# Optimization experiments

Measured on AMD Instinct MI355X. Metric: run time of the kernel, lower is better.

Reference implementation:

```python
import jax, jax.numpy as jnp
import numpy as np

N_NODES = 40000
N_EDGES = 640000
IN_FEATS = 256
EDGE_FEATS = 64
OUT_FEATS = 128
NUM_HEADS = 8
D = OUT_FEATS // NUM_HEADS  # 16


def setup_inputs() -> dict:
    key = jax.random.key(0)
    ks = jax.random.split(key, 9)
    node_feats = jax.random.normal(ks[0], (N_NODES, IN_FEATS), dtype=jnp.float32)
    edge_feats = jax.random.normal(ks[1], (N_EDGES, EDGE_FEATS), dtype=jnp.float32)
    src = jax.random.randint(ks[2], (N_EDGES,), 0, N_NODES, dtype=jnp.int32)
    dst = jax.random.randint(ks[3], (N_EDGES,), 0, N_NODES, dtype=jnp.int32)
    # learned parameters (xavier-ish scale)
    node_w = jax.random.normal(ks[4], (OUT_FEATS, IN_FEATS), dtype=jnp.float32) * (2.0 / (IN_FEATS + OUT_FEATS)) ** 0.5
    node_b = jnp.zeros((OUT_FEATS,), dtype=jnp.float32)
    edge_w = jax.random.normal(ks[5], (OUT_FEATS, EDGE_FEATS), dtype=jnp.float32) * (2.0 / (EDGE_FEATS + OUT_FEATS)) ** 0.5
    edge_b = jnp.zeros((OUT_FEATS,), dtype=jnp.float32)
    attn = jax.random.normal(ks[6], (1, NUM_HEADS, 3 * D), dtype=jnp.float32) * 0.1
    return {"node_feats": node_feats, "edge_feats": edge_feats, "src": src, "dst": dst,
            "node_w": node_w, "node_b": node_b, "edge_w": edge_w, "edge_b": edge_b, "attn": attn}


def reference(node_feats, edge_feats, src, dst, node_w, node_b, edge_w, edge_b, attn):
    N = node_feats.shape[0]
    # Node / edge projections -> [N,H,D], [E,H,D]
    Wh = (node_feats @ node_w.T + node_b).reshape(-1, NUM_HEADS, D)
    We = (edge_feats @ edge_w.T + edge_b).reshape(-1, NUM_HEADS, D)
    # Split attn into src/dst/edge parts: attn is [1,H,3D]
    a = attn[0]  # [H,3D]
    a_src, a_dst, a_e = a[:, :D], a[:, D:2 * D], a[:, 2 * D:]
    # Per-node partial scores [N,H], then gather per edge; edge part [E,H]
    s_src = jnp.einsum('nhd,hd->nh', Wh, a_src)
    s_dst = jnp.einsum('nhd,hd->nh', Wh, a_dst)
    s_e = jnp.einsum('ehd,hd->eh', We, a_e)
    e = s_src[src] + s_dst[dst] + s_e  # [E,H]
    e = jax.nn.leaky_relu(e, negative_slope=0.2)
    # Edge softmax over incoming edges of each dst node
    m = jax.ops.segment_max(e, dst, num_segments=N)          # [N,H]
    ex = jnp.exp(e - m[dst])                                  # [E,H]
    z = jax.ops.segment_sum(ex, dst, num_segments=N)          # [N,H]
    alpha = ex / z[dst]                                       # [E,H]
    # Weighted scatter-sum aggregation of source features
    msg = alpha[:, :, None] * Wh[src]                         # [E,H,D]
    h = jax.ops.segment_sum(msg, dst, num_segments=N)         # [N,H,D]
    return h.reshape(N, NUM_HEADS * D)
```

## Files before the change

### kernel.cpp

```cpp
#include <hip/hip_runtime.h>
#include <hip/hip_fp16.h>
#include <stdint.h>
#include <stddef.h>

#define N_NODES   40000
#define N_EDGES   640000
#define IN_FEATS  256
#define EDGE_FEATS 64
#define OUT_FEATS 128
#define NUM_HEADS 8
#define HD        16

typedef __attribute__((ext_vector_type(8))) short  short8;
typedef __attribute__((ext_vector_type(4))) float  floatx4;

__device__ inline short f2bf(float f) {
  union { float f; uint32_t u; } v; v.f = f;
  uint32_t r = v.u + 0x7fffu + ((v.u >> 16) & 1u);
  return (short)(r >> 16);
}

__device__ inline short8 cvt8(float4 lo, float4 hi) {
  short8 r;
  r[0] = f2bf(lo.x); r[1] = f2bf(lo.y); r[2] = f2bf(lo.z); r[3] = f2bf(lo.w);
  r[4] = f2bf(hi.x); r[5] = f2bf(hi.y); r[6] = f2bf(hi.z); r[7] = f2bf(hi.w);
  return r;
}

__device__ inline float bflo(uint32_t w) {
  union { uint32_t u; float f; } v; v.u = w << 16; return v.f;
}
__device__ inline float bfhi(uint32_t w) {
  union { uint32_t u; float f; } v; v.u = w & 0xffff0000u; return v.f;
}

__global__ __launch_bounds__(512) void prep_hist_kernel(
    const float* __restrict__ edge_w, const float* __restrict__ edge_b,
    const float* __restrict__ attn, const float* __restrict__ node_w,
    const int* __restrict__ dst,
    float* __restrict__ Wfold, float* __restrict__ bfold,
    uint32_t* __restrict__ Wbf, int* __restrict__ deg) {
  int tid = threadIdx.x;
  if (blockIdx.x == 0) {
    int h = tid >> 6, k = tid & 63;
    float s = 0.f;
    #pragma unroll
    for (int d = 0; d < HD; d++)
      s += edge_w[(h * HD + d) * EDGE_FEATS + k] * attn[h * 48 + 32 + d];
    Wfold[h * EDGE_FEATS + k] = s;
    if (k == 0) {
      float b = 0.f;
      #pragma unroll
      for (int d = 0; d < HD; d++)
        b += edge_b[h * HD + d] * attn[h * 48 + 32 + d];
      bfold[h] = b;
    }
    const float2* W2 = (const float2*)node_w;
    #pragma unroll
    for (int j = 0; j < 32; j++) {
      int p = j * 512 + tid;
      float2 f = W2[p];
      Wbf[p] = (uint32_t)(uint16_t)f2bf(f.x) |
               ((uint32_t)(uint16_t)f2bf(f.y) << 16);
    }
  } else {
    int e = (blockIdx.x - 1) * 512 + tid;
    atomicAdd(&deg[dst[e]], 1);
  }
}

__global__ __launch_bounds__(256) void wh_gemm(
    const float* __restrict__ A,
    const uint32_t* __restrict__ Wbf,
    const float* __restrict__ bias,
    uint32_t* __restrict__ Whp) {
  int wave = (blockIdx.x * blockDim.x + threadIdx.x) >> 6;
  int lane = threadIdx.x & 63;
  int m0 = wave * 16;
  if (m0 >= N_NODES) return;
  int row = lane & 15, quad = lane >> 4;

  floatx4 acc[8];
  #pragma unroll
  for (int nt = 0; nt < 8; nt++) acc[nt] = (floatx4)(0.f);

  const float4* A4 = (const float4*)A;
  const uint4*  W4 = (const uint4*)Wbf;
  int a_base = ((m0 + row) * IN_FEATS + quad * 8) >> 2;

  #pragma unroll
  for (int s = 0; s < 8; s++) {
    float4 alo = A4[a_base + s * 8];
    float4 ahi = A4[a_base + s * 8 + 1];
    short8 af = cvt8(alo, ahi);
    #pragma unroll
    for (int nt = 0; nt < 8; nt++) {
      int fo = (nt * 16 + row) * IN_FEATS + s * 32 + quad * 8;
      uint4 u = W4[fo >> 3];
      short8 bf = *(short8*)&u;
      acc[nt] = __builtin_amdgcn_mfma_f32_16x16x32_bf16(af, bf, acc[nt], 0, 0, 0);
    }
  }
  #pragma unroll
  for (int nt = 0; nt < 4; nt++) {
    float blo_ = bias[nt * 16 + row];
    float bhi_ = bias[64 + nt * 16 + row];
    #pragma unroll
    for (int r = 0; r < 4; r++) {
      int m = m0 + quad * 4 + r;
      float lo = acc[nt][r] + blo_;
      float hi = acc[nt + 4][r] + bhi_;
      uint32_t d = (uint32_t)(uint16_t)f2bf(lo) |
                   ((uint32_t)(uint16_t)f2bf(hi) << 16);
      Whp[m * 64 + nt * 16 + row] = d;
    }
  }
}

__global__ __launch_bounds__(256) void ssd_kernel(
    const uint32_t* __restrict__ Whp, const float* __restrict__ attn,
    float* __restrict__ s_src, float* __restrict__ s_dst) {
  int t = blockIdx.x * 256 + threadIdx.x;
  int n = t >> 2, hp = t & 3;
  const uint4* p = (const uint4*)(Whp + n * 64 + hp * 16);
  const float* as_lo = attn + hp * 48;
  const float* ad_lo = attn + hp * 48 + 16;
  const float* as_hi = attn + (hp + 4) * 48;
  const float* ad_hi = attn + (hp + 4) * 48 + 16;
  float ss_lo = 0.f, sd_lo = 0.f, ss_hi = 0.f, sd_hi = 0.f;
  #pragma unroll
  for (int q = 0; q < 4; q++) {
    uint4 u = p[q];
    uint32_t ws[4] = {u.x, u.y, u.z, u.w};
    #pragma unroll
    for (int k = 0; k < 4; k++) {
      int d = q * 4 + k;
      float lo = bflo(ws[k]), hi = bfhi(ws[k]);
      ss_lo += lo * as_lo[d]; sd_lo += lo * ad_lo[d];
      ss_hi += hi * as_hi[d]; sd_hi += hi * ad_hi[d];
    }
  }
  s_src[n * 8 + hp]     = ss_lo;
  s_src[n * 8 + hp + 4] = ss_hi;
  s_dst[n * 8 + hp]     = sd_lo;
  s_dst[n * 8 + hp + 4] = sd_hi;
}

__global__ __launch_bounds__(1024) void scan_kernel(
    const int* __restrict__ deg, int* __restrict__ rs, int* __restrict__ cursor) {
  __shared__ int wsum[16];
  __shared__ int carry;
  int tid = threadIdx.x;
  int lane = tid & 63, w = tid >> 6;
  if (tid == 0) carry = 0;
  __syncthreads();
  for (int chunk = 0; chunk < 40; chunk++) {
    int i = chunk * 1024 + tid;
    int v = (i < N_NODES) ? deg[i] : 0;
    int x = v;
    #pragma unroll
    for (int off = 1; off < 64; off <<= 1) {
      int y = __shfl_up(x, off, 64);
      if (lane >= off) x += y;
    }
    if (lane == 63) wsum[w] = x;
    __syncthreads();
    int p = carry, tot = 0;
    #pragma unroll
    for (int j = 0; j < 16; j++) {
      int s = wsum[j];
      if (j < w) p += s;
      tot += s;
    }
    int excl = p + x - v;
    if (i < N_NODES) { rs[i] = excl; cursor[i] = excl; }
    __syncthreads();
    if (tid == 0) carry += tot;
  }
  __syncthreads();
  if (tid == 0) rs[N_NODES] = carry;
}

__global__ __launch_bounds__(256) void edge_kernel(
    const float* __restrict__ edge_feats, const int* __restrict__ src,
    const int* __restrict__ dst, const float* __restrict__ Wfold,
    const float* __restrict__ bfold, const float* __restrict__ s_src,
    const float* __restrict__ s_dst, uint4* __restrict__ lg16) {
  int e = blockIdx.x * 256 + threadIdx.x;
  int s = src[e], d = dst[e];
  const float4* ss4 = (const float4*)(s_src + (size_t)s * 8);
  const float4* sd4 = (const float4*)(s_dst + (size_t)d * 8);
  float4 sa = ss4[0], sb = ss4[1];
  float4 da = sd4[0], db = sd4[1];

  float acc[8];
  #pragma unroll
  for (int h = 0; h < 8; h++) acc[h] = bfold[h];
  const float4* ef4 = (const float4*)(edge_feats + (size_t)e * EDGE_FEATS);
  #pragma unroll
  for (int k4 = 0; k4 < 16; k4++) {
    float4 f = ef4[k4];
    #pragma unroll
    for (int h = 0; h < 8; h++) {
      const float* wr = Wfold + h * EDGE_FEATS + k4 * 4;
      acc[h] += f.x * wr[0] + f.y * wr[1] + f.z * wr[2] + f.w * wr[3];
    }
  }
  float v[8];
  v[0] = acc[0] + sa.x + da.x; v[1] = acc[1] + sa.y + da.y;
  v[2] = acc[2] + sa.z + da.z; v[3] = acc[3] + sa.w + da.w;
  v[4] = acc[4] + sb.x + db.x; v[5] = acc[5] + sb.y + db.y;
  v[6] = acc[6] + sb.z + db.z; v[7] = acc[7] + sb.w + db.w;
  #pragma unroll
  for (int h = 0; h < 8; h++) v[h] = v[h] > 0.f ? v[h] : 0.2f * v[h];

  uint32_t pk[4];
  #pragma unroll
  for (int j = 0; j < 4; j++) {
    uint32_t lo = __half_as_ushort(__float2half_rn(v[2 * j]));
    uint32_t hi = __half_as_ushort(__float2half_rn(v[2 * j + 1]));
    pk[j] = lo | (hi << 16);
  }
  lg16[e] = make_uint4(pk[0], pk[1], pk[2], pk[3]);
}

__global__ __launch_bounds__(256) void scatter_kernel(
    const int* __restrict__ src, const int* __restrict__ dst,
    int* __restrict__ cursor, int2* __restrict__ csr8) {
  int e = blockIdx.x * 256 + threadIdx.x;
  int d = dst[e];
  int s = src[e];
  int pos = atomicAdd(&cursor[d], 1);
  csr8[pos] = make_int2(e, s);
}

__global__ __launch_bounds__(256) void aggregate_kernel(
    const int* __restrict__ rs, const int2* __restrict__ csr8,
    const uint4* __restrict__ lg16, const uint32_t* __restrict__ Whp,
    float* __restrict__ out) {
  int node = blockIdx.x * 4 + (threadIdx.x >> 6);
  int lane = threadIdx.x & 63;
  int h1 = lane >> 4;
  int start = rs[node], end = rs[node + 1];
  uint32_t sh = (h1 & 1) * 16;
  bool hi_pair = (h1 & 2) != 0;

  float z1 = 0.f, z2 = 0.f, a1 = 0.f, a2 = 0.f;

  #define STEP(g, wv)                                                  \
    {                                                                  \
      uint32_t c1 = hi_pair ? (g).y : (g).x;                           \
      uint32_t c2 = hi_pair ? (g).w : (g).z;                           \
      float l1 = __half2float(__ushort_as_half((uint16_t)(c1 >> sh))); \
      float l2 = __half2float(__ushort_as_half((uint16_t)(c2 >> sh))); \
      float e1 = __expf(l1), e2 = __expf(l2);                          \
      z1 += e1; z2 += e2;                                              \
      a1 += e1 * bflo(wv); a2 += e2 * bfhi(wv);                        \
    }

  int i = start;
  for (; i + 3 < end; i += 4) {
    int2 r0 = csr8[i], r1 = csr8[i + 1], r2 = csr8[i + 2], r3 = csr8[i + 3];
    uint4 g0 = lg16[r0.x], g1 = lg16[r1.x], g2 = lg16[r2.x], g3 = lg16[r3.x];
    uint32_t w0 = Whp[(size_t)r0.y * 64 + lane];
    uint32_t w1 = Whp[(size_t)r1.y * 64 + lane];
    uint32_t w2 = Whp[(size_t)r2.y * 64 + lane];
    uint32_t w3 = Whp[(size_t)r3.y * 64 + lane];
    STEP(g0, w0); STEP(g1, w1); STEP(g2, w2); STEP(g3, w3);
  }
  for (; i < end; i++) {
    int2 r0 = csr8[i];
    uint4 g0 = lg16[r0.x];
    uint32_t w0 = Whp[(size_t)r0.y * 64 + lane];
    STEP(g0, w0);
  }
  #undef STEP

  float o1 = (end > start) ? a1 / z1 : 0.f;
  float o2 = (end > start) ? a2 / z2 : 0.f;
  out[(size_t)node * OUT_FEATS + lane] = o1;
  out[(size_t)node * OUT_FEATS + 64 + lane] = o2;
}

extern "C" void kernel_launch(void* const* d_in, const int* in_sizes, int n_in,
                              void* d_out, int out_size, void* d_ws, size_t ws_size,
                              hipStream_t stream) {
  const float* node_feats = (const float*)d_in[0];
  const float* edge_feats = (const float*)d_in[1];
  const int*   src        = (const int*)d_in[2];
  const int*   dst        = (const int*)d_in[3];
  const float* node_w     = (const float*)d_in[4];
  const float* node_b     = (const float*)d_in[5];
  const float* edge_w     = (const float*)d_in[6];
  const float* edge_b     = (const float*)d_in[7];
  const float* attn       = (const float*)d_in[8];
  float* out = (float*)d_out;

  char* ws = (char*)d_ws;
  size_t off = 0;
  auto alloc = [&](size_t bytes) {
    void* p = ws + off;
    off += (bytes + 255) & ~(size_t)255;
    return p;
  };
  uint32_t* Whp      = (uint32_t*)alloc((size_t)N_NODES * 64 * 4);
  float*    s_src    = (float*)alloc((size_t)N_NODES * NUM_HEADS * 4);
  float*    s_dst    = (float*)alloc((size_t)N_NODES * NUM_HEADS * 4);
  uint4*    lg16     = (uint4*)alloc((size_t)N_EDGES * 16);
  int2*     csr8     = (int2*)alloc((size_t)N_EDGES * 8);
  int*      deg      = (int*)alloc((size_t)N_NODES * 4);
  int*      rs       = (int*)alloc((size_t)(N_NODES + 1) * 4);
  int*      cursor   = (int*)alloc((size_t)N_NODES * 4);
  float*    Wfold    = (float*)alloc(NUM_HEADS * EDGE_FEATS * 4);
  float*    bfold    = (float*)alloc(NUM_HEADS * 4);
  uint32_t* Wbf      = (uint32_t*)alloc((size_t)OUT_FEATS * IN_FEATS * 2);

  hipMemsetAsync(deg, 0, (size_t)N_NODES * 4, stream);

  prep_hist_kernel<<<1 + N_EDGES / 512, 512, 0, stream>>>(
      edge_w, edge_b, attn, node_w, dst, Wfold, bfold, Wbf, deg);
  wh_gemm<<<N_NODES / 16 / 4, 256, 0, stream>>>(node_feats, Wbf, node_b, Whp);
  ssd_kernel<<<N_NODES * 4 / 256, 256, 0, stream>>>(Whp, attn, s_src, s_dst);
  scan_kernel<<<1, 1024, 0, stream>>>(deg, rs, cursor);
  edge_kernel<<<N_EDGES / 256, 256, 0, stream>>>(edge_feats, src, dst, Wfold,
                                                 bfold, s_src, s_dst, lg16);
  scatter_kernel<<<N_EDGES / 256, 256, 0, stream>>>(src, dst, cursor, csr8);
  aggregate_kernel<<<N_NODES / 4, 256, 0, stream>>>(rs, csr8, lg16, Whp, out);
}
```

Measured before the change: 471.1 us.

## Fuse edge scoring with CSR scatter and parallelize scan chunk barriers

Merges the edge-logit kernel and the CSR scatter kernel, so each edge writes its packed logits and source id directly at its CSR slot. The aggregate kernel then reads logits contiguously instead of gathering them by edge id, and one kernel launch plus the edge-id indirection go away. The scan kernel is restructured to do all 40 warp-level scans first with a single barrier, then combine the partial sums per chunk, removing the per-chunk syncs. The trade-off is scattered 16-byte writes in the edge kernel in place of coalesced ones, plus more registers and shared memory in the scan.

```diff
diff --git a/kernel.cpp b/kernel.cpp
--- a/kernel.cpp
+++ b/kernel.cpp
@@ -148,46 +148,56 @@
 
 __global__ __launch_bounds__(1024) void scan_kernel(
     const int* __restrict__ deg, int* __restrict__ rs, int* __restrict__ cursor) {
-  __shared__ int wsum[16];
-  __shared__ int carry;
+  __shared__ int wsum[40][16];
   int tid = threadIdx.x;
   int lane = tid & 63, w = tid >> 6;
-  if (tid == 0) carry = 0;
+
+  int ex[40];
+  #pragma unroll
+  for (int c = 0; c < 40; c++) {
+    int i = c * 1024 + tid;
+    int vv = (i < N_NODES) ? deg[i] : 0;
+    int xv = vv;
+    #pragma unroll
+    for (int off = 1; off < 64; off <<= 1) {
+      int y = __shfl_up(xv, off, 64);
+      if (lane >= off) xv += y;
+    }
+    ex[c] = xv - vv;
+    if (lane == 63) wsum[c][w] = xv;
+  }
   __syncthreads();
-  for (int chunk = 0; chunk < 40; chunk++) {
-    int i = chunk * 1024 + tid;
-    int v = (i < N_NODES) ? deg[i] : 0;
-    int x = v;
-    #pragma unroll
-    for (int off = 1; off < 64; off <<= 1) {
-      int y = __shfl_up(x, off, 64);
-      if (lane >= off) x += y;
-    }
-    if (lane == 63) wsum[w] = x;
-    __syncthreads();
-    int p = carry, tot = 0;
+
+  int carry = 0;
+  #pragma unroll
+  for (int c = 0; c < 40; c++) {
+    int p = carry;
     #pragma unroll
     for (int j = 0; j < 16; j++) {
-      int s = wsum[j];
+      int s = wsum[c][j];
       if (j < w) p += s;
-      tot += s;
-    }
-    int excl = p + x - v;
-    if (i < N_NODES) { rs[i] = excl; cursor[i] = excl; }
-    __syncthreads();
-    if (tid == 0) carry += tot;
-  }
-  __syncthreads();
+      carry += s;
+    }
+    int i = c * 1024 + tid;
+    if (i < N_NODES) {
+      int excl = p + ex[c];
+      rs[i] = excl;
+      cursor[i] = excl;
+    }
+  }
   if (tid == 0) rs[N_NODES] = carry;
 }
 
-__global__ __launch_bounds__(256) void edge_kernel(
+__global__ __launch_bounds__(256) void edge_scatter_kernel(
     const float* __restrict__ edge_feats, const int* __restrict__ src,
     const int* __restrict__ dst, const float* __restrict__ Wfold,
     const float* __restrict__ bfold, const float* __restrict__ s_src,
-    const float* __restrict__ s_dst, uint4* __restrict__ lg16) {
+    const float* __restrict__ s_dst, int* __restrict__ cursor,
+    int* __restrict__ csrc, uint4* __restrict__ clg) {
   int e = blockIdx.x * 256 + threadIdx.x;
   int s = src[e], d = dst[e];
+  int pos = atomicAdd(&cursor[d], 1);
+
   const float4* ss4 = (const float4*)(s_src + (size_t)s * 8);
   const float4* sd4 = (const float4*)(s_dst + (size_t)d * 8);
   float4 sa = ss4[0], sb = ss4[1];
@@ -221,22 +231,13 @@
     uint32_t hi = __half_as_ushort(__float2half_rn(v[2 * j + 1]));
     pk[j] = lo | (hi << 16);
   }
-  lg16[e] = make_uint4(pk[0], pk[1], pk[2], pk[3]);
-}
-
-__global__ __launch_bounds__(256) void scatter_kernel(
-    const int* __restrict__ src, const int* __restrict__ dst,
-    int* __restrict__ cursor, int2* __restrict__ csr8) {
-  int e = blockIdx.x * 256 + threadIdx.x;
-  int d = dst[e];
-  int s = src[e];
-  int pos = atomicAdd(&cursor[d], 1);
-  csr8[pos] = make_int2(e, s);
+  csrc[pos] = s;
+  clg[pos] = make_uint4(pk[0], pk[1], pk[2], pk[3]);
 }
 
 __global__ __launch_bounds__(256) void aggregate_kernel(
-    const int* __restrict__ rs, const int2* __restrict__ csr8,
-    const uint4* __restrict__ lg16, const uint32_t* __restrict__ Whp,
+    const int* __restrict__ rs, const int* __restrict__ csrc,
+    const uint4* __restrict__ clg, const uint32_t* __restrict__ Whp,
     float* __restrict__ out) {
   int node = blockIdx.x * 4 + (threadIdx.x >> 6);
   int lane = threadIdx.x & 63;
@@ -260,18 +261,18 @@
 
   int i = start;
   for (; i + 3 < end; i += 4) {
-    int2 r0 = csr8[i], r1 = csr8[i + 1], r2 = csr8[i + 2], r3 = csr8[i + 3];
-    uint4 g0 = lg16[r0.x], g1 = lg16[r1.x], g2 = lg16[r2.x], g3 = lg16[r3.x];
-    uint32_t w0 = Whp[(size_t)r0.y * 64 + lane];
-    uint32_t w1 = Whp[(size_t)r1.y * 64 + lane];
-    uint32_t w2 = Whp[(size_t)r2.y * 64 + lane];
-    uint32_t w3 = Whp[(size_t)r3.y * 64 + lane];
+    int s0 = csrc[i], s1 = csrc[i + 1], s2 = csrc[i + 2], s3 = csrc[i + 3];
+    uint4 g0 = clg[i], g1 = clg[i + 1], g2 = clg[i + 2], g3 = clg[i + 3];
+    uint32_t w0 = Whp[(size_t)s0 * 64 + lane];
+    uint32_t w1 = Whp[(size_t)s1 * 64 + lane];
+    uint32_t w2 = Whp[(size_t)s2 * 64 + lane];
+    uint32_t w3 = Whp[(size_t)s3 * 64 + lane];
     STEP(g0, w0); STEP(g1, w1); STEP(g2, w2); STEP(g3, w3);
   }
   for (; i < end; i++) {
-    int2 r0 = csr8[i];
-    uint4 g0 = lg16[r0.x];
-    uint32_t w0 = Whp[(size_t)r0.y * 64 + lane];
+    int s0 = csrc[i];
+    uint4 g0 = clg[i];
+    uint32_t w0 = Whp[(size_t)s0 * 64 + lane];
     STEP(g0, w0);
   }
   #undef STEP
@@ -306,8 +307,8 @@
   uint32_t* Whp      = (uint32_t*)alloc((size_t)N_NODES * 64 * 4);
   float*    s_src    = (float*)alloc((size_t)N_NODES * NUM_HEADS * 4);
   float*    s_dst    = (float*)alloc((size_t)N_NODES * NUM_HEADS * 4);
-  uint4*    lg16     = (uint4*)alloc((size_t)N_EDGES * 16);
-  int2*     csr8     = (int2*)alloc((size_t)N_EDGES * 8);
+  int*      csrc     = (int*)alloc((size_t)N_EDGES * 4);
+  uint4*    clg      = (uint4*)alloc((size_t)N_EDGES * 16);
   int*      deg      = (int*)alloc((size_t)N_NODES * 4);
   int*      rs       = (int*)alloc((size_t)(N_NODES + 1) * 4);
   int*      cursor   = (int*)alloc((size_t)N_NODES * 4);
@@ -322,8 +323,7 @@
   wh_gemm<<<N_NODES / 16 / 4, 256, 0, stream>>>(node_feats, Wbf, node_b, Whp);
   ssd_kernel<<<N_NODES * 4 / 256, 256, 0, stream>>>(Whp, attn, s_src, s_dst);
   scan_kernel<<<1, 1024, 0, stream>>>(deg, rs, cursor);
-  edge_kernel<<<N_EDGES / 256, 256, 0, stream>>>(edge_feats, src, dst, Wfold,
-                                                 bfold, s_src, s_dst, lg16);
-  scatter_kernel<<<N_EDGES / 256, 256, 0, stream>>>(src, dst, cursor, csr8);
-  aggregate_kernel<<<N_NODES / 4, 256, 0, stream>>>(rs, csr8, lg16, Whp, out);
-}
+  edge_scatter_kernel<<<N_EDGES / 256, 256, 0, stream>>>(
+      edge_feats, src, dst, Wfold, bfold, s_src, s_dst, cursor, csrc, clg);
+  aggregate_kernel<<<N_NODES / 4, 256, 0, stream>>>(rs, csrc, clg, Whp, out);
+}
```

Measured after the change: 437.1 us. 1.08x faster.
